# Kernel optimization log

Hardware: AMD Instinct MI355X
Metric: run time of the kernel (lower is better)

## Reference

```python
import jax, jax.numpy as jnp
import numpy as np

G = 4          # group_dim
MIN_R = 0.2    # min_radius
MAX_R = 2.0    # max_radius


def _bilinear_sample(fea, x, y):
    """PyTorch grid_sample(mode='bilinear', padding_mode='zeros', align_corners=True).
    fea: (B,C,H,W); x,y: (B,N) absolute pixel coords. Returns (B,C,N)."""
    B, C, H, W = fea.shape
    x0 = jnp.floor(x)
    y0 = jnp.floor(y)
    feaf = fea.reshape(B, C, H * W)

    def gather(xi, yi):
        valid = (xi >= 0) & (xi <= W - 1) & (yi >= 0) & (yi <= H - 1)
        xc = jnp.clip(xi, 0, W - 1).astype(jnp.int32)
        yc = jnp.clip(yi, 0, H - 1).astype(jnp.int32)
        v = jnp.take_along_axis(feaf, (yc * W + xc)[:, None, :], axis=2)
        return jnp.where(valid[:, None, :], v, 0.0)

    wx = (x - x0)[:, None, :]
    wy = (y - y0)[:, None, :]
    return (gather(x0, y0) * (1 - wx) * (1 - wy)
            + gather(x0 + 1, y0) * wx * (1 - wy)
            + gather(x0, y0 + 1) * (1 - wx) * wy
            + gather(x0 + 1, y0 + 1) * wx * wy)


def _warp(src_fea, src_proj, ref_proj, depth):
    """differentiable_warping: homography warp of src_fea per depth sample.
    src_fea (B,C,H,W), projs (B,4,4), depth (B,D,H,W) -> (B,C,D,H,W)."""
    B, C, H, W = src_fea.shape
    D = depth.shape[1]
    proj = jnp.einsum('bij,bjk->bik', src_proj, jnp.linalg.inv(ref_proj))
    rot = proj[:, :3, :3]
    trans = proj[:, :3, 3]
    yy, xx = jnp.meshgrid(jnp.arange(H, dtype=jnp.float32),
                          jnp.arange(W, dtype=jnp.float32), indexing='ij')
    xyz = jnp.stack([xx.ravel(), yy.ravel(), jnp.ones(H * W, dtype=jnp.float32)], 0)  # (3,HW)
    rot_xyz = jnp.einsum('bij,jn->bin', rot, xyz)  # (B,3,HW)
    pts = rot_xyz[:, :, None, :] * depth.reshape(B, 1, D, H * W) + trans[:, :, None, None]
    z = pts[:, 2]
    z = jnp.where(z == 0, 1e-8, z)
    # grid is computed under torch.no_grad in the original -> stop_gradient
    px = jax.lax.stop_gradient(pts[:, 0] / z).reshape(B, D * H * W)
    py = jax.lax.stop_gradient(pts[:, 1] / z).reshape(B, D * H * W)
    return _bilinear_sample(src_fea, px, py).reshape(B, C, D, H, W)


def _make_proj(pm):
    # pm (B,2,4,4): [.,0]=extrinsic, [.,1]=intrinsic; K[:3,:3] @ E[:3,:4]
    top = jnp.einsum('bij,bjk->bik', pm[:, 1, :3, :3], pm[:, 0, :3, :4])
    return pm[:, 0].at[:, :3, :4].set(top)


def _forward(inverse_depth, features, proj_matrices, view_weights, confidence,
             depth_interval, depth_max, depth_min, CostNum):
    ref_fea = features[0]
    B, C, H, W = ref_fea.shape
    D = CostNum
    # get_cur_depth_range_samples (confidence branch)
    cur = inverse_depth[:, 0]                     # (B,H,W)
    radius = (D // 2) * depth_interval
    radius = MIN_R * radius + (1.0 - confidence) * (MAX_R - MIN_R) * radius
    dmin = cur - radius
    interval = 2.0 * radius / (D - 1)             # (dmax - dmin)/(D-1)
    samples = jnp.clip(jnp.arange(D, dtype=jnp.float32).reshape(1, D, 1, 1)
                       * interval[:, None] + dmin[:, None], 0.0, 1.0)  # (B,D,H,W)
    # disp_to_depth
    min_disp = 1.0 / depth_max
    max_disp = 1.0 / depth_min
    depth = 1.0 / jnp.maximum(min_disp + (max_disp - min_disp) * samples, 1e-6)
    ref_proj = _make_proj(proj_matrices[:, 0])
    ref_vol = ref_fea.reshape(B, G, C // G, 1, H, W)
    vw_sum = 1e-8
    cor_feats = 0.0
    for i in range(features.shape[0] - 1):        # fixed small number of source views
        src_proj = _make_proj(proj_matrices[:, i + 1])
        warped = _warp(features[i + 1], src_proj, ref_proj, depth)   # (B,C,D,H,W)
        cor = (warped.reshape(B, G, C // G, D, H, W) * ref_vol).mean(axis=2)  # (B,G,D,H,W)
        w = view_weights[:, i][:, None, None]     # (B,1,1,H,W)
        vw_sum = vw_sum + w
        cor_feats = cor_feats + w * cor
    cor_feats = cor_feats / vw_sum
    return cor_feats.reshape(B, G * D, H, W), samples


def setup_inputs():
    key = jax.random.key(0)
    k1, k2, k3, k4 = jax.random.split(key, 4)
    B, V, C, H, W = 2, 5, 32, 256, 320
    features = jax.random.normal(k1, (V, B, C, H, W), dtype=jnp.float32)
    inverse_depth = jax.random.uniform(k2, (B, 1, H, W), dtype=jnp.float32)
    view_weights = jax.random.uniform(k3, (B, V - 1, H, W), dtype=jnp.float32)
    confidence = jax.random.uniform(k4, (B, H, W), dtype=jnp.float32)
    # realistic camera matrices
    K = np.eye(4, dtype=np.float32)
    K[0, 0] = K[1, 1] = 0.8 * W
    K[0, 2] = W / 2.0
    K[1, 2] = H / 2.0
    proj = np.zeros((B, V, 2, 4, 4), dtype=np.float32)
    for v in range(V):
        E = np.eye(4, dtype=np.float32)
        a = 0.05 * v
        E[0, 0] = np.cos(a); E[0, 2] = np.sin(a)
        E[2, 0] = -np.sin(a); E[2, 2] = np.cos(a)
        E[0, 3] = 0.1 * v
        proj[:, v, 0] = E
        proj[:, v, 1] = K
    return {"inverse_depth": inverse_depth, "features": features,
            "proj_matrices": jnp.asarray(proj), "view_weights": view_weights,
            "confidence": confidence, "depth_interval": jnp.float32(0.02),
            "depth_max": jnp.float32(10.0), "depth_min": jnp.float32(0.5),
            "CostNum": 4}


def reference(inverse_depth, features, proj_matrices, view_weights, confidence,
              depth_interval, depth_max, depth_min, CostNum):
    return _forward(inverse_depth, features, proj_matrices, view_weights, confidence,
                    depth_interval, depth_max, depth_min, CostNum)
```

## Files before the change

kernel.cpp:

```cpp
#include <hip/hip_runtime.h>

#define Bsz 2
#define Vn  5
#define Cn  32
#define Gg  4
#define Hh  256
#define Ww  320
#define Dd  4
#define HWp (Hh*Ww)

#define NVB ((Vn-1)*Bsz)
#define T_OFFSET 512
#define T_BYTES ((size_t)NVB * HWp * (Cn/2) * sizeof(unsigned int))

typedef _Float16 half2v __attribute__((ext_vector_type(2)));

__device__ __forceinline__ float dot2h(unsigned int a, half2v b, float c) {
    return __builtin_amdgcn_fdot2(__builtin_bit_cast(half2v, a), b, c, false);
}

__global__ void setup_rt(const float* __restrict__ pm, float* __restrict__ RT) {
    int b = threadIdx.x;
    if (b >= Bsz) return;

    float P[Vn][16];
    for (int v = 0; v < Vn; ++v) {
        const float* E = pm + ((b * Vn + v) * 2 + 0) * 16;
        const float* K = pm + ((b * Vn + v) * 2 + 1) * 16;
        for (int i = 0; i < 3; ++i)
            for (int j = 0; j < 4; ++j) {
                float s = 0.f;
                for (int k = 0; k < 3; ++k) s += K[i * 4 + k] * E[k * 4 + j];
                P[v][i * 4 + j] = s;
            }
        for (int j = 0; j < 4; ++j) P[v][12 + j] = E[12 + j];
    }

    float A[4][8];
    for (int i = 0; i < 4; ++i)
        for (int j = 0; j < 4; ++j) {
            A[i][j] = P[0][i * 4 + j];
            A[i][4 + j] = (i == j) ? 1.f : 0.f;
        }
    for (int col = 0; col < 4; ++col) {
        int piv = col;
        float best = fabsf(A[col][col]);
        for (int r = col + 1; r < 4; ++r) {
            float v = fabsf(A[r][col]);
            if (v > best) { best = v; piv = r; }
        }
        if (piv != col)
            for (int j = 0; j < 8; ++j) {
                float t = A[col][j]; A[col][j] = A[piv][j]; A[piv][j] = t;
            }
        float inv = 1.f / A[col][col];
        for (int j = 0; j < 8; ++j) A[col][j] *= inv;
        for (int r = 0; r < 4; ++r)
            if (r != col) {
                float f = A[r][col];
                for (int j = 0; j < 8; ++j) A[r][j] -= f * A[col][j];
            }
    }
    float inv0[16];
    for (int i = 0; i < 4; ++i)
        for (int j = 0; j < 4; ++j) inv0[i * 4 + j] = A[i][4 + j];

    for (int i2 = 0; i2 < Vn - 1; ++i2) {
        const float* Ps = P[i2 + 1];
        float M[12];
        for (int i = 0; i < 3; ++i)
            for (int j = 0; j < 4; ++j) {
                float s = 0.f;
                for (int k = 0; k < 4; ++k) s += Ps[i * 4 + k] * inv0[k * 4 + j];
                M[i * 4 + j] = s;
            }
        float* o = RT + (b * (Vn - 1) + i2) * 12;
        o[0] = M[0];  o[1] = M[1];  o[2] = M[2];
        o[3] = M[4];  o[4] = M[5];  o[5] = M[6];
        o[6] = M[8];  o[7] = M[9];  o[8] = M[10];
        o[9] = M[3];  o[10] = M[7]; o[11] = M[11];
    }
}

__global__ __launch_bounds__(256) void transpose_src_fp16(
    const float* __restrict__ features, unsigned int* __restrict__ T)
{
    int tid = blockIdx.x * blockDim.x + threadIdx.x;
    if (tid >= NVB * HWp) return;
    int p  = tid % HWp;
    int vb = tid / HWp;

    const float* src = features + (size_t)(vb + Bsz) * Cn * HWp + p;
    float v[Cn];
    #pragma unroll
    for (int c = 0; c < Cn; ++c) v[c] = src[(size_t)c * HWp];

    uint4* dst = (uint4*)(T + ((size_t)vb * HWp + p) * (Cn / 2));
    #pragma unroll
    for (int q = 0; q < Cn / 8; ++q) {
        uint4 o;
        half2v p0 = { (_Float16)v[8*q + 0], (_Float16)v[8*q + 1] };
        half2v p1 = { (_Float16)v[8*q + 2], (_Float16)v[8*q + 3] };
        half2v p2 = { (_Float16)v[8*q + 4], (_Float16)v[8*q + 5] };
        half2v p3 = { (_Float16)v[8*q + 6], (_Float16)v[8*q + 7] };
        o.x = __builtin_bit_cast(unsigned int, p0);
        o.y = __builtin_bit_cast(unsigned int, p1);
        o.z = __builtin_bit_cast(unsigned int, p2);
        o.w = __builtin_bit_cast(unsigned int, p3);
        dst[q] = o;
    }
}

__global__ __launch_bounds__(256, 2) void getcost_fast(
    const float* __restrict__ inv_depth,
    const float* __restrict__ features,
    const float* __restrict__ view_weights,
    const float* __restrict__ confidence,
    const float* __restrict__ sc_interval,
    const float* __restrict__ sc_dmax,
    const float* __restrict__ sc_dmin,
    const float* __restrict__ RT,
    const unsigned int* __restrict__ T,
    float* __restrict__ out)
{
    int tid = blockIdx.x * blockDim.x + threadIdx.x;
    int g    = tid & 3;
    int rest = tid >> 2;
    int p = rest % HWp;
    int b = rest / HWp;
    int h = p / Ww;
    int w = p % Ww;

    float dI    = sc_interval[0];
    float dmaxv = sc_dmax[0];
    float dminv = sc_dmin[0];

    float cur  = inv_depth[b * HWp + p];
    float conf = confidence[b * HWp + p];
    float radius0 = (float)(Dd / 2) * dI;
    float radius  = 0.2f * radius0 + (1.0f - conf) * 1.8f * radius0;
    float dmin_   = cur - radius;
    float interval = 2.0f * radius / (float)(Dd - 1);
    float min_disp = 1.0f / dmaxv;
    float max_disp = 1.0f / dminv;

    float sample[Dd], depth[Dd];
    #pragma unroll
    for (int d = 0; d < Dd; ++d) {
        float s = (float)d * interval + dmin_;
        s = fminf(fmaxf(s, 0.0f), 1.0f);
        sample[d] = s;
        depth[d] = 1.0f / fmaxf(min_disp + (max_disp - min_disp) * s, 1e-6f);
    }

    half2v rp[4];
    {
        const float* reff = features + (size_t)b * Cn * HWp + (size_t)(g * 8) * HWp + p;
        #pragma unroll
        for (int j = 0; j < 4; ++j) {
            half2v pr = { (_Float16)reff[(size_t)(2*j)   * HWp],
                          (_Float16)reff[(size_t)(2*j+1) * HWp] };
            rp[j] = pr;
        }
    }

    float acc[Dd] = {0.f, 0.f, 0.f, 0.f};
    float vw_sum = 1e-8f;
    float xf = (float)w, yf = (float)h;

    #pragma unroll
    for (int i = 0; i < Vn - 1; ++i) {
        const float* rt = RT + (b * (Vn - 1) + i) * 12;
        float rx = rt[0] * xf + rt[1] * yf + rt[2];
        float ry = rt[3] * xf + rt[4] * yf + rt[5];
        float rz = rt[6] * xf + rt[7] * yf + rt[8];
        float t0 = rt[9], t1 = rt[10], t2 = rt[11];
        float wvw = view_weights[((size_t)(b * (Vn - 1) + i)) * HWp + p];
        vw_sum += wvw;
        float wv8 = wvw * 0.125f;

        const unsigned int* tvg = T + (size_t)(i * Bsz + b) * HWp * (Cn / 2) + g * 4;

        float cww[Dd][4];
        int   cox[Dd][4];
        #pragma unroll
        for (int d = 0; d < Dd; ++d) {
            float dep = depth[d];
            float ptx = rx * dep + t0;
            float pty = ry * dep + t1;
            float ptz = rz * dep + t2;
            if (ptz == 0.0f) ptz = 1e-8f;
            float rcz = __builtin_amdgcn_rcpf(ptz);
            float px = ptx * rcz, py = pty * rcz;

            float x0 = floorf(px), y0 = floorf(py);
            float wx = px - x0,   wy = py - y0;
            float x1 = x0 + 1.0f, y1 = y0 + 1.0f;
            bool vx0 = (x0 >= 0.f) && (x0 <= (float)(Ww - 1));
            bool vx1 = (x1 >= 0.f) && (x1 <= (float)(Ww - 1));
            bool vy0 = (y0 >= 0.f) && (y0 <= (float)(Hh - 1));
            bool vy1 = (y1 >= 0.f) && (y1 <= (float)(Hh - 1));
            int ix0 = (int)fminf(fmaxf(x0, 0.f), (float)(Ww - 1));
            int ix1 = (int)fminf(fmaxf(x1, 0.f), (float)(Ww - 1));
            int iy0 = (int)fminf(fmaxf(y0, 0.f), (float)(Hh - 1));
            int iy1 = (int)fminf(fmaxf(y1, 0.f), (float)(Hh - 1));
            cww[d][0] = ((vx0 && vy0) ? (1.f - wx) * (1.f - wy) : 0.f) * wv8;
            cww[d][1] = ((vx1 && vy0) ? wx * (1.f - wy) : 0.f) * wv8;
            cww[d][2] = ((vx0 && vy1) ? (1.f - wx) * wy : 0.f) * wv8;
            cww[d][3] = ((vx1 && vy1) ? wx * wy : 0.f) * wv8;
            cox[d][0] = iy0 * Ww + ix0; cox[d][1] = iy0 * Ww + ix1;
            cox[d][2] = iy1 * Ww + ix0; cox[d][3] = iy1 * Ww + ix1;
        }

        uint4 uu[Dd][4];
        #pragma unroll
        for (int d = 0; d < Dd; ++d)
            #pragma unroll
            for (int k = 0; k < 4; ++k)
                uu[d][k] = *(const uint4*)(tvg + (size_t)cox[d][k] * (Cn / 2));

        #pragma unroll
        for (int d = 0; d < Dd; ++d) {
            #pragma unroll
            for (int k = 0; k < 4; ++k) {
                float t = dot2h(uu[d][k].x, rp[0], 0.0f);
                t = dot2h(uu[d][k].y, rp[1], t);
                t = dot2h(uu[d][k].z, rp[2], t);
                t = dot2h(uu[d][k].w, rp[3], t);
                acc[d] += cww[d][k] * t;
            }
        }
    }

    float invvw = 1.0f / vw_sum;
    size_t outbase = (size_t)b * Gg * Dd * HWp;
    #pragma unroll
    for (int d = 0; d < Dd; ++d)
        out[outbase + (size_t)(g * Dd + d) * HWp + p] = acc[d] * invvw;
    if (g == 0) {
        size_t sbase = (size_t)Bsz * Gg * Dd * HWp + (size_t)b * Dd * HWp + p;
        #pragma unroll
        for (int d = 0; d < Dd; ++d)
            out[sbase + (size_t)d * HWp] = sample[d];
    }
}

__global__ __launch_bounds__(256) void getcost_main(
    const float* __restrict__ inv_depth,
    const float* __restrict__ features,
    const float* __restrict__ view_weights,
    const float* __restrict__ confidence,
    const float* __restrict__ sc_interval,
    const float* __restrict__ sc_dmax,
    const float* __restrict__ sc_dmin,
    const float* __restrict__ RT,
    float* __restrict__ out)
{
    int tid = blockIdx.x * blockDim.x + threadIdx.x;
    if (tid >= Bsz * Dd * HWp) return;
    int p  = tid % HWp;
    int bd = tid / HWp;
    int d  = bd % Dd;
    int b  = bd / Dd;
    int h  = p / Ww;
    int w  = p % Ww;

    float dI    = sc_interval[0];
    float dmaxv = sc_dmax[0];
    float dminv = sc_dmin[0];

    float cur  = inv_depth[b * HWp + p];
    float conf = confidence[b * HWp + p];
    float radius0 = (float)(Dd / 2) * dI;
    float radius  = 0.2f * radius0 + (1.0f - conf) * 1.8f * radius0;
    float dmin_   = cur - radius;
    float interval = 2.0f * radius / (float)(Dd - 1);
    float sample = (float)d * interval + dmin_;
    sample = fminf(fmaxf(sample, 0.0f), 1.0f);
    float min_disp = 1.0f / dmaxv;
    float max_disp = 1.0f / dminv;
    float depth = 1.0f / fmaxf(min_disp + (max_disp - min_disp) * sample, 1e-6f);

    float ref[Cn];
    const float* reff = features + (size_t)b * Cn * HWp + p;
    #pragma unroll
    for (int c = 0; c < Cn; ++c) ref[c] = reff[(size_t)c * HWp];

    float acc[Gg] = {0.f, 0.f, 0.f, 0.f};
    float vw_sum = 1e-8f;
    float xf = (float)w, yf = (float)h;

    #pragma unroll
    for (int i = 0; i < Vn - 1; ++i) {
        const float* rt = RT + (b * (Vn - 1) + i) * 12;
        float rx = rt[0] * xf + rt[1] * yf + rt[2];
        float ry = rt[3] * xf + rt[4] * yf + rt[5];
        float rz = rt[6] * xf + rt[7] * yf + rt[8];
        float wvw = view_weights[((size_t)(b * (Vn - 1) + i)) * HWp + p];
        vw_sum += wvw;

        float ptx = rx * depth + rt[9];
        float pty = ry * depth + rt[10];
        float ptz = rz * depth + rt[11];
        if (ptz == 0.0f) ptz = 1e-8f;
        float px = ptx / ptz, py = pty / ptz;

        float x0 = floorf(px), y0 = floorf(py);
        float wx = px - x0,   wy = py - y0;
        float x1 = x0 + 1.0f, y1 = y0 + 1.0f;
        bool vx0 = (x0 >= 0.f) && (x0 <= (float)(Ww - 1));
        bool vx1 = (x1 >= 0.f) && (x1 <= (float)(Ww - 1));
        bool vy0 = (y0 >= 0.f) && (y0 <= (float)(Hh - 1));
        bool vy1 = (y1 >= 0.f) && (y1 <= (float)(Hh - 1));
        int ix0 = (int)fminf(fmaxf(x0, 0.f), (float)(Ww - 1));
        int ix1 = (int)fminf(fmaxf(x1, 0.f), (float)(Ww - 1));
        int iy0 = (int)fminf(fmaxf(y0, 0.f), (float)(Hh - 1));
        int iy1 = (int)fminf(fmaxf(y1, 0.f), (float)(Hh - 1));
        float w00 = (vx0 && vy0) ? (1.f - wx) * (1.f - wy) : 0.f;
        float w10 = (vx1 && vy0) ? wx * (1.f - wy) : 0.f;
        float w01 = (vx0 && vy1) ? (1.f - wx) * wy : 0.f;
        float w11 = (vx1 && vy1) ? wx * wy : 0.f;
        int o00 = iy0 * Ww + ix0, o10 = iy0 * Ww + ix1;
        int o01 = iy1 * Ww + ix0, o11 = iy1 * Ww + ix1;

        const float* src = features + (size_t)((i + 1) * Bsz + b) * Cn * HWp;
        float wv8 = wvw * 0.125f;
        #pragma unroll
        for (int c = 0; c < Cn; ++c) {
            const float* sc = src + (size_t)c * HWp;
            float v = w00 * sc[o00] + w10 * sc[o10] + w01 * sc[o01] + w11 * sc[o11];
            acc[c >> 3] += v * ref[c] * wv8;
        }
    }

    float invvw = 1.0f / vw_sum;
    size_t outbase = (size_t)b * Gg * Dd * HWp;
    #pragma unroll
    for (int g = 0; g < Gg; ++g)
        out[outbase + (size_t)(g * Dd + d) * HWp + p] = acc[g] * invvw;
    out[(size_t)Bsz * Gg * Dd * HWp + (size_t)(b * Dd + d) * HWp + p] = sample;
}

extern "C" void kernel_launch(void* const* d_in, const int* in_sizes, int n_in,
                              void* d_out, int out_size, void* d_ws, size_t ws_size,
                              hipStream_t stream) {
    const float* inv_depth = (const float*)d_in[0];
    const float* features  = (const float*)d_in[1];
    const float* pm        = (const float*)d_in[2];
    const float* vw        = (const float*)d_in[3];
    const float* conf      = (const float*)d_in[4];
    const float* dI        = (const float*)d_in[5];
    const float* dmax      = (const float*)d_in[6];
    const float* dmin      = (const float*)d_in[7];
    float* RT = (float*)d_ws;

    hipLaunchKernelGGL(setup_rt, dim3(1), dim3(64), 0, stream, pm, RT);

    bool has_ws = (ws_size >= T_OFFSET + T_BYTES);

    if (has_ws) {
        unsigned int* T = (unsigned int*)((char*)d_ws + T_OFFSET);
        int ttot = NVB * HWp;
        hipLaunchKernelGGL(transpose_src_fp16, dim3((ttot + 255) / 256), dim3(256), 0,
                           stream, features, T);
        int total = Bsz * HWp * Gg;
        hipLaunchKernelGGL(getcost_fast, dim3(total / 256), dim3(256), 0, stream,
                           inv_depth, features, vw, conf, dI, dmax, dmin, RT, T,
                           (float*)d_out);
    } else {
        int total = Bsz * Dd * HWp;
        hipLaunchKernelGGL(getcost_main, dim3((total + 255) / 256), dim3(256), 0, stream,
                           inv_depth, features, vw, conf, dI, dmax, dmin, RT,
                           (float*)d_out);
    }
}
```

Before: 68.65 us.

## Stage per-block source footprint in LDS for bilinear gathers in cost kernel

Each 128-thread block now covers a 16x2 pixel tile. Per view, the block reduces the bounding box of all bilinear taps with wave shuffles plus a shared-memory step. If the box fits in 256 records, the block copies that region of the fp16 transposed source into LDS cooperatively and then gathers from LDS. Otherwise it falls back to direct global gathers. This aims to cut redundant global and L2 traffic from neighbouring pixels reading overlapping texels, at the cost of extra barriers, a non-unrolled view loop and a possibly wasteful bounding-box load when depths spread widely.

After: 82.99 us. 1.21x slower.

```diff
diff --git a/kernel.cpp b/kernel.cpp
--- a/kernel.cpp
+++ b/kernel.cpp
@@ -12,6 +12,12 @@
 #define NVB ((Vn-1)*Bsz)
 #define T_OFFSET 512
 #define T_BYTES ((size_t)NVB * HWp * (Cn/2) * sizeof(unsigned int))
+
+#define TPW 16
+#define TPH 2
+#define PIXB (TPW*TPH)
+#define THREADS 128
+#define TILE_REC 256
 
 typedef _Float16 half2v __attribute__((ext_vector_type(2)));
 
@@ -111,7 +117,7 @@
     }
 }
 
-__global__ __launch_bounds__(256, 2) void getcost_fast(
+__global__ __launch_bounds__(THREADS, 4) void getcost_lds(
     const float* __restrict__ inv_depth,
     const float* __restrict__ features,
     const float* __restrict__ view_weights,
@@ -123,13 +129,22 @@
     const unsigned int* __restrict__ T,
     float* __restrict__ out)
 {
-    int tid = blockIdx.x * blockDim.x + threadIdx.x;
-    int g    = tid & 3;
-    int rest = tid >> 2;
-    int p = rest % HWp;
-    int b = rest / HWp;
-    int h = p / Ww;
-    int w = p % Ww;
+    __shared__ unsigned int tile[TILE_REC * 16];
+    __shared__ int red[8];
+
+    int t = threadIdx.x;
+    int g = t & 3;
+    int pixloc = t >> 2;
+    int blk = blockIdx.x;
+    const int TPR = Ww / TPW;
+    const int TPI = TPR * (Hh / TPH);
+    int b  = blk / TPI;
+    int tb = blk - b * TPI;
+    int ty = tb / TPR;
+    int tx = tb - ty * TPR;
+    int w = tx * TPW + (pixloc & (TPW - 1));
+    int h = ty * TPH + (pixloc >> 4);
+    int p = h * Ww + w;
 
     float dI    = sc_interval[0];
     float dmaxv = sc_dmax[0];
@@ -168,7 +183,7 @@
     float vw_sum = 1e-8f;
     float xf = (float)w, yf = (float)h;
 
-    #pragma unroll
+    #pragma unroll 1
     for (int i = 0; i < Vn - 1; ++i) {
         const float* rt = RT + (b * (Vn - 1) + i) * 12;
         float rx = rt[0] * xf + rt[1] * yf + rt[2];
@@ -179,10 +194,9 @@
         vw_sum += wvw;
         float wv8 = wvw * 0.125f;
 
-        const unsigned int* tvg = T + (size_t)(i * Bsz + b) * HWp * (Cn / 2) + g * 4;
-
         float cww[Dd][4];
-        int   cox[Dd][4];
+        int xp[Dd], yp[Dd];
+        int xlo = Ww - 1, xhi = 0, ylo = Hh - 1, yhi = 0;
         #pragma unroll
         for (int d = 0; d < Dd; ++d) {
             float dep = depth[d];
@@ -208,26 +222,89 @@
             cww[d][1] = ((vx1 && vy0) ? wx * (1.f - wy) : 0.f) * wv8;
             cww[d][2] = ((vx0 && vy1) ? (1.f - wx) * wy : 0.f) * wv8;
             cww[d][3] = ((vx1 && vy1) ? wx * wy : 0.f) * wv8;
-            cox[d][0] = iy0 * Ww + ix0; cox[d][1] = iy0 * Ww + ix1;
-            cox[d][2] = iy1 * Ww + ix0; cox[d][3] = iy1 * Ww + ix1;
-        }
-
-        uint4 uu[Dd][4];
+            xp[d] = ix0 | (ix1 << 16);
+            yp[d] = iy0 | (iy1 << 16);
+            xlo = min(xlo, ix0); xhi = max(xhi, ix1);
+            ylo = min(ylo, iy0); yhi = max(yhi, iy1);
+        }
+
         #pragma unroll
-        for (int d = 0; d < Dd; ++d)
+        for (int m = 4; m <= 32; m <<= 1) {
+            xlo = min(xlo, __shfl_xor(xlo, m));
+            xhi = max(xhi, __shfl_xor(xhi, m));
+            ylo = min(ylo, __shfl_xor(ylo, m));
+            yhi = max(yhi, __shfl_xor(yhi, m));
+        }
+        __syncthreads();
+        if ((t & 63) == 0) {
+            int w4 = (t >> 6) * 4;
+            red[w4 + 0] = xlo; red[w4 + 1] = xhi;
+            red[w4 + 2] = ylo; red[w4 + 3] = yhi;
+        }
+        __syncthreads();
+        xlo = min(red[0], red[4]); xhi = max(red[1], red[5]);
+        ylo = min(red[2], red[6]); yhi = max(red[3], red[7]);
+        int TW = xhi - xlo + 1;
+        int area = TW * (yhi - ylo + 1);
+
+        const unsigned int* tv = T + (size_t)(i * Bsz + b) * HWp * (Cn / 2);
+
+        if (area <= TILE_REC) {
+            int total16 = area * 4;
+            for (int c = t; c < total16; c += THREADS) {
+                int rec = c >> 2, sub = c & 3;
+                int rrow = rec / TW;
+                int rcol = rec - rrow * TW;
+                *(uint4*)&tile[(rec << 4) + (sub << 2)] =
+                    *(const uint4*)(tv + (size_t)((ylo + rrow) * Ww + xlo + rcol) * (Cn / 2)
+                                       + (sub << 2));
+            }
+            __syncthreads();
             #pragma unroll
-            for (int k = 0; k < 4; ++k)
-                uu[d][k] = *(const uint4*)(tvg + (size_t)cox[d][k] * (Cn / 2));
-
-        #pragma unroll
-        for (int d = 0; d < Dd; ++d) {
+            for (int d = 0; d < Dd; ++d) {
+                int ix0 = xp[d] & 0xffff, ix1 = xp[d] >> 16;
+                int iy0 = yp[d] & 0xffff, iy1 = yp[d] >> 16;
+                int dx  = ix1 - ix0;
+                int i00 = (iy0 - ylo) * TW + (ix0 - xlo);
+                int i01 = (iy1 - ylo) * TW + (ix0 - xlo);
+                uint4 u0 = *(const uint4*)&tile[(i00 << 4) + (g << 2)];
+                uint4 u1 = *(const uint4*)&tile[((i00 + dx) << 4) + (g << 2)];
+                uint4 u2 = *(const uint4*)&tile[(i01 << 4) + (g << 2)];
+                uint4 u3 = *(const uint4*)&tile[((i01 + dx) << 4) + (g << 2)];
+                float s0 = dot2h(u0.x, rp[0], 0.f); s0 = dot2h(u0.y, rp[1], s0);
+                s0 = dot2h(u0.z, rp[2], s0);        s0 = dot2h(u0.w, rp[3], s0);
+                float s1 = dot2h(u1.x, rp[0], 0.f); s1 = dot2h(u1.y, rp[1], s1);
+                s1 = dot2h(u1.z, rp[2], s1);        s1 = dot2h(u1.w, rp[3], s1);
+                float s2 = dot2h(u2.x, rp[0], 0.f); s2 = dot2h(u2.y, rp[1], s2);
+                s2 = dot2h(u2.z, rp[2], s2);        s2 = dot2h(u2.w, rp[3], s2);
+                float s3 = dot2h(u3.x, rp[0], 0.f); s3 = dot2h(u3.y, rp[1], s3);
+                s3 = dot2h(u3.z, rp[2], s3);        s3 = dot2h(u3.w, rp[3], s3);
+                acc[d] += cww[d][0] * s0 + cww[d][1] * s1
+                        + cww[d][2] * s2 + cww[d][3] * s3;
+            }
+        } else {
+            __syncthreads();
+            const unsigned int* tvg = tv + g * 4;
             #pragma unroll
-            for (int k = 0; k < 4; ++k) {
-                float t = dot2h(uu[d][k].x, rp[0], 0.0f);
-                t = dot2h(uu[d][k].y, rp[1], t);
-                t = dot2h(uu[d][k].z, rp[2], t);
-                t = dot2h(uu[d][k].w, rp[3], t);
-                acc[d] += cww[d][k] * t;
+            for (int d = 0; d < Dd; ++d) {
+                int ix0 = xp[d] & 0xffff, ix1 = xp[d] >> 16;
+                int iy0 = yp[d] & 0xffff, iy1 = yp[d] >> 16;
+                int c00 = iy0 * Ww + ix0, c10 = iy0 * Ww + ix1;
+                int c01 = iy1 * Ww + ix0, c11 = iy1 * Ww + ix1;
+                uint4 u0 = *(const uint4*)(tvg + (size_t)c00 * (Cn / 2));
+                uint4 u1 = *(const uint4*)(tvg + (size_t)c10 * (Cn / 2));
+                uint4 u2 = *(const uint4*)(tvg + (size_t)c01 * (Cn / 2));
+                uint4 u3 = *(const uint4*)(tvg + (size_t)c11 * (Cn / 2));
+                float s0 = dot2h(u0.x, rp[0], 0.f); s0 = dot2h(u0.y, rp[1], s0);
+                s0 = dot2h(u0.z, rp[2], s0);        s0 = dot2h(u0.w, rp[3], s0);
+                float s1 = dot2h(u1.x, rp[0], 0.f); s1 = dot2h(u1.y, rp[1], s1);
+                s1 = dot2h(u1.z, rp[2], s1);        s1 = dot2h(u1.w, rp[3], s1);
+                float s2 = dot2h(u2.x, rp[0], 0.f); s2 = dot2h(u2.y, rp[1], s2);
+                s2 = dot2h(u2.z, rp[2], s2);        s2 = dot2h(u2.w, rp[3], s2);
+                float s3 = dot2h(u3.x, rp[0], 0.f); s3 = dot2h(u3.y, rp[1], s3);
+                s3 = dot2h(u3.z, rp[2], s3);        s3 = dot2h(u3.w, rp[3], s3);
+                acc[d] += cww[d][0] * s0 + cww[d][1] * s1
+                        + cww[d][2] * s2 + cww[d][3] * s3;
             }
         }
     }
@@ -363,8 +440,8 @@
         int ttot = NVB * HWp;
         hipLaunchKernelGGL(transpose_src_fp16, dim3((ttot + 255) / 256), dim3(256), 0,
                            stream, features, T);
-        int total = Bsz * HWp * Gg;
-        hipLaunchKernelGGL(getcost_fast, dim3(total / 256), dim3(256), 0, stream,
+        int nblk = Bsz * HWp / PIXB;
+        hipLaunchKernelGGL(getcost_lds, dim3(nblk), dim3(THREADS), 0, stream,
                            inv_depth, features, vw, conf, dI, dmax, dmin, RT, T,
                            (float*)d_out);
     } else {
```
